# Kernel optimization log

Hardware: AMD Instinct MI355X
Metric: run time of the kernel (lower is better)

The kernel has to match this reference:

```python
import jax, jax.numpy as jnp
import numpy as np

EMBED_DIM = 1024
B, S = 4, 2048
SCALE = float(np.sqrt(EMBED_DIM))


def setup_inputs() -> dict:
    key = jax.random.key(0)
    ks = jax.random.split(key, 9)
    d = EMBED_DIM
    init = 1.0 / np.sqrt(d)
    return {
        "query": jax.random.normal(ks[0], (B, S, d), jnp.float32),
        "key": jax.random.normal(ks[1], (B, S, d), jnp.float32),
        "value": jax.random.normal(ks[2], (B, S, d), jnp.float32),
        "wq": jax.random.uniform(ks[3], (d, d), jnp.float32, -init, init),
        "bq": jax.random.uniform(ks[4], (d,), jnp.float32, -init, init),
        "wk": jax.random.uniform(ks[5], (d, d), jnp.float32, -init, init),
        "bk": jax.random.uniform(ks[6], (d,), jnp.float32, -init, init),
        "wv": jax.random.uniform(ks[7], (d, d), jnp.float32, -init, init),
        "bv": jax.random.uniform(ks[8], (d,), jnp.float32, -init, init),
    }


def reference(query, key, value, wq, bq, wk, bk, wv, bv):
    # Linear projections (torch Linear: x @ W^T + b; here weights stored as [in, out])
    q = query @ wq + bq            # [B,S,D]
    k = key @ wk + bk              # [B,S,D]
    v = value @ wv + bv            # [B,S,D]
    scores = jnp.einsum("bqd,bkd->bqk", q, k) / SCALE   # [B,S,S]
    attn = jax.nn.softmax(scores, axis=-1)
    # dropout in eval mode -> identity
    return jnp.einsum("bqk,bkd->bqd", attn, v)          # [B,S,D]
```

## Files before the change

### kernel.cpp

```cpp
#include <hip/hip_runtime.h>
#include <hip/hip_bf16.h>

typedef __attribute__((ext_vector_type(4))) float   f32x4;
typedef __attribute__((ext_vector_type(8))) __bf16  bf16x8;
typedef __attribute__((ext_vector_type(4))) __bf16  bf16x4;

#define NB 4
#define SS 2048
#define DD 1024

__device__ __forceinline__ void gload_lds16(const void* g, void* l) {
  __builtin_amdgcn_global_load_lds((const __attribute__((address_space(1))) void*)g,
                                   (__attribute__((address_space(3))) void*)l,
                                   16, 0, 0);
}

__global__ __launch_bounds__(256) void cvt_in_kernel(
    const float* __restrict__ q, const float* __restrict__ k,
    const float* __restrict__ v, __bf16* __restrict__ X)
{
  const float* src = blockIdx.z == 0 ? q : (blockIdx.z == 1 ? k : v);
  __bf16* dst = X + (size_t)blockIdx.z * (size_t)(NB * SS * DD);
  size_t i = ((size_t)blockIdx.x * 256 + threadIdx.x) * 4;
  float4 f = *(const float4*)&src[i];
  bf16x4 o = { (__bf16)f.x, (__bf16)f.y, (__bf16)f.z, (__bf16)f.w };
  *(bf16x4*)&dst[i] = o;
}

__global__ __launch_bounds__(256) void prep_w_kernel(
    const float* __restrict__ wq, const float* __restrict__ wk, const float* __restrict__ wv,
    const float* __restrict__ bq, const float* __restrict__ bk, const float* __restrict__ bv,
    __bf16* __restrict__ Wt, float* __restrict__ biasbuf)
{
  const int z = blockIdx.z;
  const float* W  = z == 0 ? wq : (z == 1 ? wk : wv);
  const float* bi = z == 0 ? bq : (z == 1 ? bk : bv);
  __bf16* dst = Wt + (size_t)z * (size_t)(DD * DD);
  const int n0 = blockIdx.x * 32, k0 = blockIdx.y * 32;
  __shared__ float t[32][33];
  const int tx = threadIdx.x & 31, ty = threadIdx.x >> 5;
  #pragma unroll
  for (int i = 0; i < 4; i++)
    t[ty + 8 * i][tx] = W[(size_t)(k0 + ty + 8 * i) * DD + n0 + tx];
  __syncthreads();
  #pragma unroll
  for (int i = 0; i < 4; i++)
    dst[(size_t)(n0 + ty + 8 * i) * DD + k0 + tx] = (__bf16)t[tx][ty + 8 * i];
  if (blockIdx.x == 0 && blockIdx.y == 0) {
    #pragma unroll
    for (int i = 0; i < 4; i++)
      biasbuf[z * DD + threadIdx.x + 256 * i] = bi[threadIdx.x + 256 * i];
  }
}

__global__ __launch_bounds__(256) void transpose_v_kernel(
    const __bf16* __restrict__ V, __bf16* __restrict__ Vt)
{
  const int b = blockIdx.z;
  const int d0 = blockIdx.x * 32, s0 = blockIdx.y * 32;
  __shared__ __bf16 t[32][34];
  const int tx = threadIdx.x & 31, ty = threadIdx.x >> 5;
  const __bf16* src = V + ((size_t)b * SS + s0) * DD + d0;
  #pragma unroll
  for (int i = 0; i < 4; i++)
    t[ty + 8 * i][tx] = src[(size_t)(ty + 8 * i) * DD + tx];
  __syncthreads();
  __bf16* dst = Vt + ((size_t)b * DD + d0) * SS + s0;
  #pragma unroll
  for (int i = 0; i < 4; i++)
    dst[(size_t)(ty + 8 * i) * SS + tx] = t[tx][ty + 8 * i];
}


#define A_OFF(BUF, MH) (((BUF)*2 + (MH)) * 16384)
#define B_OFF(BUF, NH) (65536 + ((BUF)*2 + (NH)) * 16384)

#define STAGE_A(BUF, MH, T) do { int t_ = (T); if (t_ >= NT) t_ = 0;            \
  const __bf16* gs_ = Ablk + (size_t)(MH) * (64 * (size_t)lda) + (size_t)t_ * 64; \
  gload_lds16(gs_ + aoff0, smem + A_OFF(BUF, MH) + tid * 16);                    \
  gload_lds16(gs_ + aoff1, smem + A_OFF(BUF, MH) + 8192 + tid * 16); } while (0)

#define STAGE_B(BUF, NH, T) do { int t_ = (T); if (t_ >= NT) t_ = 0;            \
  const __bf16* gs_ = Bblk + (size_t)(NH) * (32 * (size_t)ldb) + (size_t)t_ * 64; \
  gload_lds16(gs_ + boff0, smem + B_OFF(BUF, NH) + tid * 16);                    \
  gload_lds16(gs_ + boff1, smem + B_OFF(BUF, NH) + 8192 + tid * 16); } while (0)

#define DSREAD_A(DST, BUF, MH)                                                  \
  _Pragma("unroll") for (int mi = 0; mi < 4; ++mi) {                            \
    _Pragma("unroll") for (int ks = 0; ks < 2; ++ks)                            \
      DST[mi][ks] = *(const bf16x8*)(smem + A_OFF(BUF, MH) + arb[ks] + mi * 2048); }

#define DSREAD_B(DST, BUF, NH)                                                  \
  _Pragma("unroll") for (int ni = 0; ni < 2; ++ni) {                            \
    _Pragma("unroll") for (int ks = 0; ks < 2; ++ks)                            \
      DST[ni][ks] = *(const bf16x8*)(smem + B_OFF(BUF, NH) + brb[ks] + ni * 2048); }

#define BARRIER_MFMA(AF, BF, MH, NH) do {                                       \
  __builtin_amdgcn_s_barrier();                                                 \
  asm volatile("s_waitcnt lgkmcnt(0)" ::: "memory");                            \
  __builtin_amdgcn_sched_barrier(0);                                            \
  __builtin_amdgcn_s_setprio(1);                                                \
  _Pragma("unroll") for (int mi = 0; mi < 4; ++mi)                              \
  _Pragma("unroll") for (int ni = 0; ni < 2; ++ni)                              \
  _Pragma("unroll") for (int ks = 0; ks < 2; ++ks)                              \
    acc[(MH)*4+mi][(NH)*2+ni] = __builtin_amdgcn_mfma_f32_16x16x32_bf16(        \
        AF[mi][ks], BF[ni][ks], acc[(MH)*4+mi][(NH)*2+ni], 0, 0, 0);            \
  __builtin_amdgcn_s_setprio(0);                                                \
  __builtin_amdgcn_sched_barrier(0);                                            \
  __builtin_amdgcn_s_barrier(); } while (0)

template <int EPI>
__global__ __launch_bounds__(512) void gemm8p_kernel(
    const __bf16* __restrict__ A, const __bf16* __restrict__ B,
    float scale, void* __restrict__ Cout,
    int K, int lda, int ldb, int ldc,
    long strideA, long strideB, long strideC)
{
  extern __shared__ char smem[];

  const int gx = gridDim.x, gy = gridDim.y;
  const int nwg = gx * gy * gridDim.z;
  int lin = blockIdx.x + gx * (blockIdx.y + gy * blockIdx.z);
  const int cpx = nwg >> 3;
  int swz = (lin & 7) * cpx + (lin >> 3);
  const int bx = swz % gx;
  int rem = swz / gx;
  const int by = rem % gy;
  const int bz = rem / gy;

  const long brow = (long)by * 256, bcol = (long)bx * 256;
  const __bf16* Ablk = A + (size_t)bz * strideA + (size_t)brow * lda;
  const __bf16* Bblk = B + (size_t)bz * strideB + (size_t)bcol * ldb;

  const int tid  = threadIdx.x;
  const int lane = tid & 63;
  const int wid  = tid >> 6;
  const int wm = wid >> 2, wn = wid & 3;
  const int l15 = lane & 15, l4 = lane >> 4;
  const int lx = (lane & 7) << 4;

  const int NT = K >> 6;
  const int niter = NT >> 1;

  int aoff0, aoff1, boff0, boff1;
  #pragma unroll
  for (int i = 0; i < 2; ++i) {
    const int p = i * 8192 + tid * 16;
    const int l = p ^ (((p >> 7) & 7) << 4);
    const int r = p >> 7;
    const int kb = l & 127;
    const int av = ((r >> 6) * 128 + (r & 63)) * lda + (kb >> 1);
    const int bv = ((r >> 5) * 64 + (r & 31)) * ldb + (kb >> 1);
    if (i == 0) { aoff0 = av; boff0 = bv; } else { aoff1 = av; boff1 = bv; }
  }

  int arb[2], brb[2];
  #pragma unroll
  for (int ks = 0; ks < 2; ++ks) {
    arb[ks] = ((((wm * 64 + l15) * 64 + l4 * 8) * 2) + ks * 64) ^ lx;
    brb[ks] = ((((wn * 32 + l15) * 64 + l4 * 8) * 2) + ks * 64) ^ lx;
  }

  f32x4 acc[8][4] = {};
  bf16x8 a0[4][2], a1[4][2], b0[2][2], b1[2][2];

  STAGE_B(0, 0, 0); STAGE_A(0, 0, 0); STAGE_A(0, 1, 0); STAGE_B(0, 1, 0);
  STAGE_B(1, 0, 1); STAGE_A(1, 0, 1);
  asm volatile("s_waitcnt vmcnt(4)" ::: "memory");
  __builtin_amdgcn_s_barrier();

  for (int it = 0; it < niter; ++it) {
    const int tt = it * 2;
    DSREAD_A(a0, 0, 0); DSREAD_B(b0, 0, 0);
    STAGE_A(1, 1, tt + 1);
    BARRIER_MFMA(a0, b0, 0, 0);
    DSREAD_A(a1, 0, 1);
    STAGE_B(1, 1, tt + 1);
    BARRIER_MFMA(a1, b0, 1, 0);
    DSREAD_B(b1, 0, 1);
    STAGE_B(0, 0, tt + 2);
    BARRIER_MFMA(a0, b1, 0, 1);
    STAGE_A(0, 0, tt + 2);
    asm volatile("s_waitcnt vmcnt(4)" ::: "memory");
    BARRIER_MFMA(a1, b1, 1, 1);
    DSREAD_A(a0, 1, 0); DSREAD_B(b0, 1, 0);
    STAGE_A(0, 1, tt + 2);
    BARRIER_MFMA(a0, b0, 0, 0);
    DSREAD_A(a1, 1, 1);
    STAGE_B(0, 1, tt + 2);
    BARRIER_MFMA(a1, b0, 1, 0);
    DSREAD_B(b1, 1, 1);
    STAGE_B(1, 0, tt + 3);
    BARRIER_MFMA(a0, b1, 0, 1);
    STAGE_A(1, 0, tt + 3);
    asm volatile("s_waitcnt vmcnt(4)" ::: "memory");
    BARRIER_MFMA(a1, b1, 1, 1);
  }

  const int cr = l4 * 4;
  __bf16* C = (__bf16*)Cout + (size_t)bz * strideC;
  #pragma unroll
  for (int m = 0; m < 8; ++m) {
    #pragma unroll
    for (int n = 0; n < 4; ++n) {
      const long row = brow + wm * 128 + m * 16 + cr;
      const long col = bcol + wn * 64 + n * 16 + l15;
      #pragma unroll
      for (int e = 0; e < 4; ++e)
        C[(row + e) * (size_t)ldc + col] = (__bf16)__expf(acc[m][n][e] * scale);
    }
  }
}


#define A2_OFF(BUF)      ((BUF) * 16384)
#define B2_OFF(BUF, NH)  (32768 + ((BUF)*2 + (NH)) * 16384)

#define STAGE_SA(BUF, T) do { int t_ = (T); if (t_ >= NT) t_ = 0;              \
  const __bf16* gA_ = Ablk + (size_t)t_ * 64;                                   \
  gload_lds16(gA_ + aoff0, smem + A2_OFF(BUF) + tid * 16);                      \
  gload_lds16(gA_ + aoff1, smem + A2_OFF(BUF) + 8192 + tid * 16);               \
  const __bf16* gB_ = Bblk + (size_t)t_ * 64;                                   \
  gload_lds16(gB_ + boff0, smem + B2_OFF(BUF, 0) + tid * 16);                   \
  gload_lds16(gB_ + boff1, smem + B2_OFF(BUF, 0) + 8192 + tid * 16); } while (0)

#define STAGE_SB(BUF, T) do { int t_ = (T); if (t_ >= NT) t_ = 0;              \
  const __bf16* gB_ = Bblk + (size_t)(128 * (size_t)ldb) + (size_t)t_ * 64;     \
  gload_lds16(gB_ + boff0, smem + B2_OFF(BUF, 1) + tid * 16);                   \
  gload_lds16(gB_ + boff1, smem + B2_OFF(BUF, 1) + 8192 + tid * 16); } while (0)

#define DSREAD_A2(BUF)                                                          \
  _Pragma("unroll") for (int mi = 0; mi < 4; ++mi) {                            \
    _Pragma("unroll") for (int ks = 0; ks < 2; ++ks)                            \
      af[mi][ks] = *(const bf16x8*)(smem + A2_OFF(BUF) + ara[ks] + mi * 2048); }

#define DSREAD_B2(DST, BUF, NH)                                                 \
  _Pragma("unroll") for (int ni = 0; ni < 2; ++ni) {                            \
    _Pragma("unroll") for (int ks = 0; ks < 2; ++ks)                            \
      DST[ni][ks] = *(const bf16x8*)(smem + B2_OFF(BUF, NH) + brb2[ks] + ni * 2048); }

#define MFMA2(BF, NH, DOSUM) do {                                               \
  __builtin_amdgcn_s_barrier();                                                 \
  asm volatile("s_waitcnt lgkmcnt(0)" ::: "memory");                            \
  __builtin_amdgcn_sched_barrier(0);                                            \
  __builtin_amdgcn_s_setprio(1);                                                \
  _Pragma("unroll") for (int mi = 0; mi < 4; ++mi)                              \
  _Pragma("unroll") for (int ni = 0; ni < 2; ++ni)                              \
  _Pragma("unroll") for (int ks = 0; ks < 2; ++ks)                              \
    acc[mi][(NH)*2+ni] = __builtin_amdgcn_mfma_f32_16x16x32_bf16(               \
        af[mi][ks], BF[ni][ks], acc[mi][(NH)*2+ni], 0, 0, 0);                   \
  if constexpr (EPI == 2) { if (DOSUM) {                                        \
    _Pragma("unroll") for (int mi = 0; mi < 4; ++mi)                            \
    _Pragma("unroll") for (int ks = 0; ks < 2; ++ks)                            \
      accs[mi] = __builtin_amdgcn_mfma_f32_16x16x32_bf16(                       \
          af[mi][ks], onesf, accs[mi], 0, 0, 0); } }                            \
  __builtin_amdgcn_s_setprio(0);                                                \
  __builtin_amdgcn_sched_barrier(0);                                            \
  __builtin_amdgcn_s_barrier(); } while (0)

template <int EPI>
__global__ __launch_bounds__(512) void gemm128_kernel(
    const __bf16* __restrict__ A, const __bf16* __restrict__ B,
    const float* __restrict__ bias, void* __restrict__ Cout,
    int K, int lda, int ldb, int ldc,
    long strideA, long strideB, long strideC)
{
  extern __shared__ char smem[];

  const int gx = gridDim.x, gy = gridDim.y;
  const int nwg = gx * gy * gridDim.z;
  int lin = blockIdx.x + gx * (blockIdx.y + gy * blockIdx.z);
  const int cpx = nwg >> 3;
  int swz = (lin & 7) * cpx + (lin >> 3);
  const int bx = swz % gx;
  int rem = swz / gx;
  const int by = rem % gy;
  const int bz = rem / gy;

  const long brow = (long)by * 128, bcol = (long)bx * 256;
  const __bf16* Ablk = A + (size_t)bz * strideA + (size_t)brow * lda;
  const __bf16* Bblk = B + (size_t)bz * strideB + (size_t)bcol * ldb;

  const int tid  = threadIdx.x;
  const int lane = tid & 63;
  const int wid  = tid >> 6;
  const int wm = wid >> 2, wn = wid & 3;
  const int l15 = lane & 15, l4 = lane >> 4;
  const int lx = (lane & 7) << 4;

  const int NT = K >> 6;
  const int niter = NT >> 1;

  int aoff0, aoff1, boff0, boff1;
  #pragma unroll
  for (int i = 0; i < 2; ++i) {
    const int p = i * 8192 + tid * 16;
    const int r = p >> 7;
    const int kb = (p ^ ((r & 7) << 4)) & 127;
    const int av = r * lda + (kb >> 1);
    const int bv = r * ldb + (kb >> 1);
    if (i == 0) { aoff0 = av; boff0 = bv; } else { aoff1 = av; boff1 = bv; }
  }

  int ara[2], brb2[2];
  #pragma unroll
  for (int ks = 0; ks < 2; ++ks) {
    ara[ks]  = ((((wm * 64 + l15) * 64 + l4 * 8) * 2) + ks * 64) ^ lx;
    brb2[ks] = ((((wn * 32 + l15) * 64 + l4 * 8) * 2) + ks * 64) ^ lx;
  }

  f32x4 acc[4][4] = {};
  f32x4 accs[4] = {};
  bf16x8 af[4][2], b0[2][2], b1[2][2];
  bf16x8 onesf;
  #pragma unroll
  for (int j = 0; j < 8; ++j) onesf[j] = (__bf16)1.0f;

  STAGE_SA(0, 0); STAGE_SB(0, 0); STAGE_SA(1, 1);
  asm volatile("s_waitcnt vmcnt(6)" ::: "memory");
  __builtin_amdgcn_s_barrier();

  for (int it = 0; it < niter; ++it) {
    const int tt = it * 2;
    STAGE_SB(1, tt + 1);
    asm volatile("s_waitcnt vmcnt(6)" ::: "memory");
    DSREAD_A2(0); DSREAD_B2(b0, 0, 0);
    MFMA2(b0, 0, 1);
    STAGE_SA(0, tt + 2);
    asm volatile("s_waitcnt vmcnt(6)" ::: "memory");
    DSREAD_B2(b1, 0, 1);
    MFMA2(b1, 1, 0);
    STAGE_SB(0, tt + 2);
    asm volatile("s_waitcnt vmcnt(6)" ::: "memory");
    DSREAD_A2(1); DSREAD_B2(b0, 1, 0);
    MFMA2(b0, 0, 1);
    STAGE_SA(1, tt + 3);
    asm volatile("s_waitcnt vmcnt(6)" ::: "memory");
    DSREAD_B2(b1, 1, 1);
    MFMA2(b1, 1, 0);
  }

  if constexpr (EPI == 2) {
    float* C = (float*)Cout + (size_t)bz * strideC;
    #pragma unroll
    for (int mi = 0; mi < 4; ++mi) {
      f32x4 inv;
      #pragma unroll
      for (int e = 0; e < 4; ++e) inv[e] = 1.0f / accs[mi][e];
      #pragma unroll
      for (int n = 0; n < 4; ++n) {
        const long row = brow + wm * 64 + mi * 16 + l4 * 4;
        const long col = bcol + (n >> 1) * 128 + wn * 32 + (n & 1) * 16 + l15;
        #pragma unroll
        for (int e = 0; e < 4; ++e)
          C[(row + e) * (size_t)ldc + col] = acc[mi][n][e] * inv[e];
      }
    }
  } else {
    __bf16* C = (__bf16*)Cout + (size_t)bz * strideC;
    #pragma unroll
    for (int mi = 0; mi < 4; ++mi) {
      #pragma unroll
      for (int n = 0; n < 4; ++n) {
        const long row = brow + wm * 64 + mi * 16 + l4 * 4;
        const long col = bcol + (n >> 1) * 128 + wn * 32 + (n & 1) * 16 + l15;
        const float bvv = bias[bz * DD + col];
        #pragma unroll
        for (int e = 0; e < 4; ++e)
          C[(row + e) * (size_t)ldc + col] = (__bf16)(acc[mi][n][e] + bvv);
      }
    }
  }
}

extern "C" void kernel_launch(void* const* d_in, const int* in_sizes, int n_in,
                              void* d_out, int out_size, void* d_ws, size_t ws_size,
                              hipStream_t stream)
{
  const float* query = (const float*)d_in[0];
  const float* key   = (const float*)d_in[1];
  const float* value = (const float*)d_in[2];
  const float* wq = (const float*)d_in[3];
  const float* bq = (const float*)d_in[4];
  const float* wk = (const float*)d_in[5];
  const float* bk = (const float*)d_in[6];
  const float* wv = (const float*)d_in[7];
  const float* bv = (const float*)d_in[8];

  char* ws = (char*)d_ws;
  __bf16* Xbf     = (__bf16*)(ws + 0);
  __bf16* Wt      = (__bf16*)(ws + 50331648);
  float*  biasbuf = (float*)(ws + 56623104);
  __bf16* Qb      = (__bf16*)(ws + 56635392);
  __bf16* Kb      = (__bf16*)(ws + 73412608);
  __bf16* Vb      = (__bf16*)(ws + 90189824);
  __bf16* P       = Xbf;
  __bf16* Vt      = Qb;

  hipFuncSetAttribute((const void*)gemm8p_kernel<1>, hipFuncAttributeMaxDynamicSharedMemorySize, 131072);
  hipFuncSetAttribute((const void*)gemm128_kernel<0>, hipFuncAttributeMaxDynamicSharedMemorySize, 131072);
  hipFuncSetAttribute((const void*)gemm128_kernel<2>, hipFuncAttributeMaxDynamicSharedMemorySize, 131072);

  dim3 b256(256), b512(512);

  cvt_in_kernel<<<dim3(8192, 1, 3), b256, 0, stream>>>(query, key, value, Xbf);
  prep_w_kernel<<<dim3(32, 32, 3), b256, 0, stream>>>(wq, wk, wv, bq, bk, bv, Wt, biasbuf);

  gemm128_kernel<0><<<dim3(4, 64, 3), b512, 98304, stream>>>(
      Xbf, Wt, biasbuf, Qb,
      1024, 1024, 1024, 1024,
      8388608L, 1048576L, 8388608L);
  gemm8p_kernel<1><<<dim3(8, 8, 4), b512, 131072, stream>>>(
      Qb, Kb, 0.03125f, P,
      1024, 1024, 1024, 2048,
      2097152L, 2097152L, 4194304L);

  transpose_v_kernel<<<dim3(32, 64, 4), b256, 0, stream>>>(Vb, Vt);

  gemm128_kernel<2><<<dim3(4, 16, 4), b512, 98304, stream>>>(
      P, Vt, nullptr, d_out,
      2048, 2048, 2048, 1024,
      4194304L, 2097152L, 2097152L);

  (void)in_sizes; (void)n_in; (void)out_size; (void)ws_size;
}
```

Baseline: 182.1 us.

## Fuse fp32-to-bf16 input conversion and V transpose into projection GEMM

Adds a dedicated projection kernel that loads fp32 activations directly through registers, converts them to bf16, and writes them into LDS. This removes the separate conversion pass and its bf16 scratch buffer. The V projection epilogue writes its output already transposed, which removes the transpose kernel. This saves two launches and several full-tensor memory round trips. The trade-offs are that the A operand now goes through register-staged loads rather than direct global-to-LDS loads, and the transposed V stores are strided.

Result: faster. 172.2 us (-5.5%).

```diff
diff --git a/kernel.cpp b/kernel.cpp
--- a/kernel.cpp
+++ b/kernel.cpp
@@ -13,18 +13,6 @@
   __builtin_amdgcn_global_load_lds((const __attribute__((address_space(1))) void*)g,
                                    (__attribute__((address_space(3))) void*)l,
                                    16, 0, 0);
-}
-
-__global__ __launch_bounds__(256) void cvt_in_kernel(
-    const float* __restrict__ q, const float* __restrict__ k,
-    const float* __restrict__ v, __bf16* __restrict__ X)
-{
-  const float* src = blockIdx.z == 0 ? q : (blockIdx.z == 1 ? k : v);
-  __bf16* dst = X + (size_t)blockIdx.z * (size_t)(NB * SS * DD);
-  size_t i = ((size_t)blockIdx.x * 256 + threadIdx.x) * 4;
-  float4 f = *(const float4*)&src[i];
-  bf16x4 o = { (__bf16)f.x, (__bf16)f.y, (__bf16)f.z, (__bf16)f.w };
-  *(bf16x4*)&dst[i] = o;
 }
 
 __global__ __launch_bounds__(256) void prep_w_kernel(
@@ -53,22 +41,173 @@
   }
 }
 
-__global__ __launch_bounds__(256) void transpose_v_kernel(
-    const __bf16* __restrict__ V, __bf16* __restrict__ Vt)
+#define A2_OFF(BUF)      ((BUF) * 16384)
+#define B2_OFF(BUF, NH)  (32768 + ((BUF)*2 + (NH)) * 16384)
+
+#define DSREAD_A2(BUF)                                                          \
+  _Pragma("unroll") for (int mi = 0; mi < 4; ++mi) {                            \
+    _Pragma("unroll") for (int ks = 0; ks < 2; ++ks)                            \
+      af[mi][ks] = *(const bf16x8*)(smem + A2_OFF(BUF) + ara[ks] + mi * 2048); }
+
+#define DSREAD_B2(DST, BUF, NH)                                                 \
+  _Pragma("unroll") for (int ni = 0; ni < 2; ++ni) {                            \
+    _Pragma("unroll") for (int ks = 0; ks < 2; ++ks)                            \
+      DST[ni][ks] = *(const bf16x8*)(smem + B2_OFF(BUF, NH) + brb2[ks] + ni * 2048); }
+
+
+#define PJ_GLA(V0, V1, V2, V3, T) do { int t_ = (T); if (t_ >= 16) t_ = 0;      \
+  const float* g_ = Ablk + (size_t)t_ * 64;                                     \
+  V0 = *(const float4*)(g_ + aoffF0); V1 = *(const float4*)(g_ + aoffF0 + 4);   \
+  V2 = *(const float4*)(g_ + aoffF1); V3 = *(const float4*)(g_ + aoffF1 + 4);   \
+  __builtin_amdgcn_sched_barrier(0); } while (0)
+
+#define PJ_WRA(BUF, V0, V1, V2, V3) do {                                        \
+  bf16x8 w0_, w1_;                                                              \
+  w0_[0]=(__bf16)V0.x; w0_[1]=(__bf16)V0.y; w0_[2]=(__bf16)V0.z; w0_[3]=(__bf16)V0.w; \
+  w0_[4]=(__bf16)V1.x; w0_[5]=(__bf16)V1.y; w0_[6]=(__bf16)V1.z; w0_[7]=(__bf16)V1.w; \
+  w1_[0]=(__bf16)V2.x; w1_[1]=(__bf16)V2.y; w1_[2]=(__bf16)V2.z; w1_[3]=(__bf16)V2.w; \
+  w1_[4]=(__bf16)V3.x; w1_[5]=(__bf16)V3.y; w1_[6]=(__bf16)V3.z; w1_[7]=(__bf16)V3.w; \
+  *(bf16x8*)(smem + A2_OFF(BUF) + tid * 16) = w0_;                              \
+  *(bf16x8*)(smem + A2_OFF(BUF) + 8192 + tid * 16) = w1_; } while (0)
+
+#define PJ_SB0(BUF, T) do { int t_ = (T); if (t_ >= 16) t_ = 0;                 \
+  const __bf16* gB_ = Bblk + (size_t)t_ * 64;                                   \
+  gload_lds16(gB_ + boff0, smem + B2_OFF(BUF, 0) + tid * 16);                   \
+  gload_lds16(gB_ + boff1, smem + B2_OFF(BUF, 0) + 8192 + tid * 16); } while (0)
+
+#define PJ_SB1(BUF, T) do { int t_ = (T); if (t_ >= 16) t_ = 0;                 \
+  const __bf16* gB_ = Bblk + (size_t)(128 * 1024) + (size_t)t_ * 64;            \
+  gload_lds16(gB_ + boff0, smem + B2_OFF(BUF, 1) + tid * 16);                   \
+  gload_lds16(gB_ + boff1, smem + B2_OFF(BUF, 1) + 8192 + tid * 16); } while (0)
+
+#define PJ_MFMA(BF, NH) do {                                                    \
+  __builtin_amdgcn_s_barrier();                                                 \
+  asm volatile("s_waitcnt lgkmcnt(0)" ::: "memory");                            \
+  __builtin_amdgcn_sched_barrier(0);                                            \
+  __builtin_amdgcn_s_setprio(1);                                                \
+  _Pragma("unroll") for (int mi = 0; mi < 4; ++mi)                              \
+  _Pragma("unroll") for (int ni = 0; ni < 2; ++ni)                              \
+  _Pragma("unroll") for (int ks = 0; ks < 2; ++ks)                              \
+    acc[mi][(NH)*2+ni] = __builtin_amdgcn_mfma_f32_16x16x32_bf16(               \
+        af[mi][ks], BF[ni][ks], acc[mi][(NH)*2+ni], 0, 0, 0);                   \
+  __builtin_amdgcn_s_setprio(0);                                                \
+  __builtin_amdgcn_sched_barrier(0);                                            \
+  __builtin_amdgcn_s_barrier(); } while (0)
+
+__global__ __launch_bounds__(512) void proj_kernel(
+    const float* __restrict__ Xq, const float* __restrict__ Xk, const float* __restrict__ Xv,
+    const __bf16* __restrict__ Wt, const float* __restrict__ bias,
+    __bf16* __restrict__ Qo, __bf16* __restrict__ Ko, __bf16* __restrict__ Vt)
 {
-  const int b = blockIdx.z;
-  const int d0 = blockIdx.x * 32, s0 = blockIdx.y * 32;
-  __shared__ __bf16 t[32][34];
-  const int tx = threadIdx.x & 31, ty = threadIdx.x >> 5;
-  const __bf16* src = V + ((size_t)b * SS + s0) * DD + d0;
-  #pragma unroll
-  for (int i = 0; i < 4; i++)
-    t[ty + 8 * i][tx] = src[(size_t)(ty + 8 * i) * DD + tx];
-  __syncthreads();
-  __bf16* dst = Vt + ((size_t)b * DD + d0) * SS + s0;
-  #pragma unroll
-  for (int i = 0; i < 4; i++)
-    dst[(size_t)(ty + 8 * i) * SS + tx] = t[tx][ty + 8 * i];
+  extern __shared__ char smem[];
+
+  const int gx = gridDim.x, gy = gridDim.y;
+  const int nwg = gx * gy * gridDim.z;
+  int lin = blockIdx.x + gx * (blockIdx.y + gy * blockIdx.z);
+  const int cpx = nwg >> 3;
+  int swz = (lin & 7) * cpx + (lin >> 3);
+  const int bx = swz % gx;
+  int rem = swz / gx;
+  const int by = rem % gy;
+  const int bz = rem / gy;
+
+  const long brow = (long)by * 128, bcol = (long)bx * 256;
+  const float* Xsel = bz == 0 ? Xq : (bz == 1 ? Xk : Xv);
+  const float* Ablk = Xsel + (size_t)brow * 1024;
+  const __bf16* Bblk = Wt + (size_t)bz * (DD * DD) + (size_t)bcol * 1024;
+
+  const int tid  = threadIdx.x;
+  const int lane = tid & 63;
+  const int wid  = tid >> 6;
+  const int wm = wid >> 2, wn = wid & 3;
+  const int l15 = lane & 15, l4 = lane >> 4;
+  const int lx = (lane & 7) << 4;
+
+  const int niter = 8;
+
+  int aoffF0, aoffF1, boff0, boff1;
+  #pragma unroll
+  for (int i = 0; i < 2; ++i) {
+    const int p = i * 8192 + tid * 16;
+    const int r = p >> 7;
+    const int kb = (p ^ ((r & 7) << 4)) & 127;
+    const int aF = r * 1024 + (kb >> 1);
+    const int bO = r * 1024 + (kb >> 1);
+    if (i == 0) { aoffF0 = aF; boff0 = bO; } else { aoffF1 = aF; boff1 = bO; }
+  }
+
+  int ara[2], brb2[2];
+  #pragma unroll
+  for (int ks = 0; ks < 2; ++ks) {
+    ara[ks]  = ((((wm * 64 + l15) * 64 + l4 * 8) * 2) + ks * 64) ^ lx;
+    brb2[ks] = ((((wn * 32 + l15) * 64 + l4 * 8) * 2) + ks * 64) ^ lx;
+  }
+
+  f32x4 acc[4][4] = {};
+  bf16x8 af[4][2], b0[2][2], b1[2][2];
+  float4 La0, La1, La2, La3, Lb0, Lb1, Lb2, Lb3;
+
+  PJ_GLA(La0, La1, La2, La3, 0);
+  PJ_SB0(0, 0); PJ_SB1(0, 0); PJ_SB0(1, 1);
+  PJ_GLA(Lb0, Lb1, Lb2, Lb3, 1);
+  asm volatile("s_waitcnt vmcnt(10)" ::: "memory");
+  PJ_WRA(0, La0, La1, La2, La3);
+  asm volatile("s_waitcnt vmcnt(0)" ::: "memory");
+  PJ_WRA(1, Lb0, Lb1, Lb2, Lb3);
+  asm volatile("s_waitcnt lgkmcnt(0)" ::: "memory");
+  __builtin_amdgcn_s_barrier();
+
+  for (int it = 0; it < niter; ++it) {
+    const int tt = it * 2;
+    PJ_GLA(La0, La1, La2, La3, tt + 2);
+    PJ_SB1(1, tt + 1);
+    DSREAD_A2(0); DSREAD_B2(b0, 0, 0);
+    PJ_MFMA(b0, 0);
+    asm volatile("s_waitcnt vmcnt(2)" ::: "memory");
+    PJ_WRA(0, La0, La1, La2, La3);
+    PJ_SB0(0, tt + 2);
+    DSREAD_B2(b1, 0, 1);
+    PJ_MFMA(b1, 1);
+    PJ_GLA(Lb0, Lb1, Lb2, Lb3, tt + 3);
+    PJ_SB1(0, tt + 2);
+    DSREAD_A2(1); DSREAD_B2(b0, 1, 0);
+    PJ_MFMA(b0, 0);
+    asm volatile("s_waitcnt vmcnt(2)" ::: "memory");
+    PJ_WRA(1, Lb0, Lb1, Lb2, Lb3);
+    PJ_SB0(1, tt + 3);
+    DSREAD_B2(b1, 1, 1);
+    PJ_MFMA(b1, 1);
+  }
+
+  if (bz == 2) {
+    #pragma unroll
+    for (int mi = 0; mi < 4; ++mi) {
+      #pragma unroll
+      for (int n = 0; n < 4; ++n) {
+        const long row = brow + wm * 64 + mi * 16 + l4 * 4;
+        const long col = bcol + (n >> 1) * 128 + wn * 32 + (n & 1) * 16 + l15;
+        const float bvv = bias[2 * DD + col];
+        const long bb = row >> 11, s = row & 2047;
+        bf16x4 pk = { (__bf16)(acc[mi][n][0] + bvv), (__bf16)(acc[mi][n][1] + bvv),
+                      (__bf16)(acc[mi][n][2] + bvv), (__bf16)(acc[mi][n][3] + bvv) };
+        *(bf16x4*)&Vt[bb * 2097152 + col * 2048 + s] = pk;
+      }
+    }
+  } else {
+    __bf16* C = bz == 0 ? Qo : Ko;
+    #pragma unroll
+    for (int mi = 0; mi < 4; ++mi) {
+      #pragma unroll
+      for (int n = 0; n < 4; ++n) {
+        const long row = brow + wm * 64 + mi * 16 + l4 * 4;
+        const long col = bcol + (n >> 1) * 128 + wn * 32 + (n & 1) * 16 + l15;
+        const float bvv = bias[bz * DD + col];
+        #pragma unroll
+        for (int e = 0; e < 4; ++e)
+          C[(row + e) * 1024 + col] = (__bf16)(acc[mi][n][e] + bvv);
+      }
+    }
+  }
 }
 
 
@@ -109,7 +248,6 @@
   __builtin_amdgcn_sched_barrier(0);                                            \
   __builtin_amdgcn_s_barrier(); } while (0)
 
-template <int EPI>
 __global__ __launch_bounds__(512) void gemm8p_kernel(
     const __bf16* __restrict__ A, const __bf16* __restrict__ B,
     float scale, void* __restrict__ Cout,
@@ -213,9 +351,6 @@
 }
 
 
-#define A2_OFF(BUF)      ((BUF) * 16384)
-#define B2_OFF(BUF, NH)  (32768 + ((BUF)*2 + (NH)) * 16384)
-
 #define STAGE_SA(BUF, T) do { int t_ = (T); if (t_ >= NT) t_ = 0;              \
   const __bf16* gA_ = Ablk + (size_t)t_ * 64;                                   \
   gload_lds16(gA_ + aoff0, smem + A2_OFF(BUF) + tid * 16);                      \
@@ -228,16 +363,6 @@
   const __bf16* gB_ = Bblk + (size_t)(128 * (size_t)ldb) + (size_t)t_ * 64;     \
   gload_lds16(gB_ + boff0, smem + B2_OFF(BUF, 1) + tid * 16);                   \
   gload_lds16(gB_ + boff1, smem + B2_OFF(BUF, 1) + 8192 + tid * 16); } while (0)
-
-#define DSREAD_A2(BUF)                                                          \
-  _Pragma("unroll") for (int mi = 0; mi < 4; ++mi) {                            \
-    _Pragma("unroll") for (int ks = 0; ks < 2; ++ks)                            \
-      af[mi][ks] = *(const bf16x8*)(smem + A2_OFF(BUF) + ara[ks] + mi * 2048); }
-
-#define DSREAD_B2(DST, BUF, NH)                                                 \
-  _Pragma("unroll") for (int ni = 0; ni < 2; ++ni) {                            \
-    _Pragma("unroll") for (int ks = 0; ks < 2; ++ks)                            \
-      DST[ni][ks] = *(const bf16x8*)(smem + B2_OFF(BUF, NH) + brb2[ks] + ni * 2048); }
 
 #define MFMA2(BF, NH, DOSUM) do {                                               \
   __builtin_amdgcn_s_barrier();                                                 \
@@ -249,19 +374,18 @@
   _Pragma("unroll") for (int ks = 0; ks < 2; ++ks)                              \
     acc[mi][(NH)*2+ni] = __builtin_amdgcn_mfma_f32_16x16x32_bf16(               \
         af[mi][ks], BF[ni][ks], acc[mi][(NH)*2+ni], 0, 0, 0);                   \
-  if constexpr (EPI == 2) { if (DOSUM) {                                        \
+  if (DOSUM) {                                                                  \
     _Pragma("unroll") for (int mi = 0; mi < 4; ++mi)                            \
     _Pragma("unroll") for (int ks = 0; ks < 2; ++ks)                            \
       accs[mi] = __builtin_amdgcn_mfma_f32_16x16x32_bf16(                       \
-          af[mi][ks], onesf, accs[mi], 0, 0, 0); } }                            \
+          af[mi][ks], onesf, accs[mi], 0, 0, 0); }                              \
   __builtin_amdgcn_s_setprio(0);                                                \
   __builtin_amdgcn_sched_barrier(0);                                            \
   __builtin_amdgcn_s_barrier(); } while (0)
 
-template <int EPI>
 __global__ __launch_bounds__(512) void gemm128_kernel(
     const __bf16* __restrict__ A, const __bf16* __restrict__ B,
-    const float* __restrict__ bias, void* __restrict__ Cout,
+    void* __restrict__ Cout,
     int K, int lda, int ldb, int ldc,
     long strideA, long strideB, long strideC)
 {
@@ -340,35 +464,19 @@
     MFMA2(b1, 1, 0);
   }
 
-  if constexpr (EPI == 2) {
-    float* C = (float*)Cout + (size_t)bz * strideC;
+  float* C = (float*)Cout + (size_t)bz * strideC;
+  #pragma unroll
+  for (int mi = 0; mi < 4; ++mi) {
+    f32x4 inv;
     #pragma unroll
-    for (int mi = 0; mi < 4; ++mi) {
-      f32x4 inv;
+    for (int e = 0; e < 4; ++e) inv[e] = 1.0f / accs[mi][e];
+    #pragma unroll
+    for (int n = 0; n < 4; ++n) {
+      const long row = brow + wm * 64 + mi * 16 + l4 * 4;
+      const long col = bcol + (n >> 1) * 128 + wn * 32 + (n & 1) * 16 + l15;
       #pragma unroll
-      for (int e = 0; e < 4; ++e) inv[e] = 1.0f / accs[mi][e];
-      #pragma unroll
-      for (int n = 0; n < 4; ++n) {
-        const long row = brow + wm * 64 + mi * 16 + l4 * 4;
-        const long col = bcol + (n >> 1) * 128 + wn * 32 + (n & 1) * 16 + l15;
-        #pragma unroll
-        for (int e = 0; e < 4; ++e)
-          C[(row + e) * (size_t)ldc + col] = acc[mi][n][e] * inv[e];
-      }
-    }
-  } else {
-    __bf16* C = (__bf16*)Cout + (size_t)bz * strideC;
-    #pragma unroll
-    for (int mi = 0; mi < 4; ++mi) {
-      #pragma unroll
-      for (int n = 0; n < 4; ++n) {
-        const long row = brow + wm * 64 + mi * 16 + l4 * 4;
-        const long col = bcol + (n >> 1) * 128 + wn * 32 + (n & 1) * 16 + l15;
-        const float bvv = bias[bz * DD + col];
-        #pragma unroll
-        for (int e = 0; e < 4; ++e)
-          C[(row + e) * (size_t)ldc + col] = (__bf16)(acc[mi][n][e] + bvv);
-      }
+      for (int e = 0; e < 4; ++e)
+        C[(row + e) * (size_t)ldc + col] = acc[mi][n][e] * inv[e];
     }
   }
 }
@@ -388,37 +496,31 @@
   const float* bv = (const float*)d_in[8];
 
   char* ws = (char*)d_ws;
-  __bf16* Xbf     = (__bf16*)(ws + 0);
-  __bf16* Wt      = (__bf16*)(ws + 50331648);
-  float*  biasbuf = (float*)(ws + 56623104);
-  __bf16* Qb      = (__bf16*)(ws + 56635392);
-  __bf16* Kb      = (__bf16*)(ws + 73412608);
-  __bf16* Vb      = (__bf16*)(ws + 90189824);
-  __bf16* P       = Xbf;
-  __bf16* Vt      = Qb;
-
-  hipFuncSetAttribute((const void*)gemm8p_kernel<1>, hipFuncAttributeMaxDynamicSharedMemorySize, 131072);
-  hipFuncSetAttribute((const void*)gemm128_kernel<0>, hipFuncAttributeMaxDynamicSharedMemorySize, 131072);
-  hipFuncSetAttribute((const void*)gemm128_kernel<2>, hipFuncAttributeMaxDynamicSharedMemorySize, 131072);
+  __bf16* P       = (__bf16*)(ws + 0);
+  __bf16* Wt      = (__bf16*)(ws + 33554432);
+  float*  biasbuf = (float*)(ws + 39845888);
+  __bf16* Qb      = (__bf16*)(ws + 39858176);
+  __bf16* Kb      = (__bf16*)(ws + 56635392);
+  __bf16* Vt      = (__bf16*)(ws + 73412608);
+
+  hipFuncSetAttribute((const void*)proj_kernel,    hipFuncAttributeMaxDynamicSharedMemorySize, 131072);
+  hipFuncSetAttribute((const void*)gemm8p_kernel,  hipFuncAttributeMaxDynamicSharedMemorySize, 131072);
+  hipFuncSetAttribute((const void*)gemm128_kernel, hipFuncAttributeMaxDynamicSharedMemorySize, 131072);
 
   dim3 b256(256), b512(512);
 
-  cvt_in_kernel<<<dim3(8192, 1, 3), b256, 0, stream>>>(query, key, value, Xbf);
   prep_w_kernel<<<dim3(32, 32, 3), b256, 0, stream>>>(wq, wk, wv, bq, bk, bv, Wt, biasbuf);
 
-  gemm128_kernel<0><<<dim3(4, 64, 3), b512, 98304, stream>>>(
-      Xbf, Wt, biasbuf, Qb,
-      1024, 1024, 1024, 1024,
-      8388608L, 1048576L, 8388608L);
-  gemm8p_kernel<1><<<dim3(8, 8, 4), b512, 131072, stream>>>(
+  proj_kernel<<<dim3(4, 64, 3), b512, 98304, stream>>>(
+      query, key, value, Wt, biasbuf, Qb, Kb, Vt);
+
+  gemm8p_kernel<<<dim3(8, 8, 4), b512, 131072, stream>>>(
       Qb, Kb, 0.03125f, P,
       1024, 1024, 1024, 2048,
       2097152L, 2097152L, 4194304L);
 
-  transpose_v_kernel<<<dim3(32, 64, 4), b256, 0, stream>>>(Vb, Vt);
-
-  gemm128_kernel<2><<<dim3(4, 16, 4), b512, 98304, stream>>>(
-      P, Vt, nullptr, d_out,
+  gemm128_kernel<<<dim3(4, 16, 4), b512, 98304, stream>>>(
+      P, Vt, d_out,
       2048, 2048, 2048, 1024,
       4194304L, 2097152L, 2097152L);
 
```

## Fuse V transpose into projection epilogue and use 128x128 two-block GEMM

Applied to the files above, without the earlier changes.

Replaces the 128x256 512-thread GEMM with a 128x128 256-thread kernel that uses a simple double-buffered loop and launch bounds allowing two blocks per CU. The V projection epilogue now writes its output transposed straight into the Vt buffer, which removes the separate transpose kernel and its extra read and write of V. The transposed stores are strided 8-byte writes, which may coalesce poorly, and the smaller tiles lower data reuse per block.

Result: faster. 168.9 us (-7.2%).

```diff
diff --git a/kernel.cpp b/kernel.cpp
--- a/kernel.cpp
+++ b/kernel.cpp
@@ -53,22 +53,173 @@
   }
 }
 
-__global__ __launch_bounds__(256) void transpose_v_kernel(
-    const __bf16* __restrict__ V, __bf16* __restrict__ Vt)
+
+#define G2A(BUF) ((BUF) * 16384)
+#define G2B(BUF) (32768 + (BUF) * 16384)
+
+#define G2_STAGE(BUF, T) do { int t_ = (T); if (t_ >= NT) t_ = 0;               \
+  const __bf16* gA_ = Ablk + (size_t)t_ * 64;                                   \
+  const __bf16* gB_ = Bblk + (size_t)t_ * 64;                                   \
+  gload_lds16(gA_ + o0, smem + G2A(BUF) + tid * 16);                            \
+  gload_lds16(gA_ + o1, smem + G2A(BUF) + 4096 + tid * 16);                     \
+  gload_lds16(gA_ + o2, smem + G2A(BUF) + 8192 + tid * 16);                     \
+  gload_lds16(gA_ + o3, smem + G2A(BUF) + 12288 + tid * 16);                    \
+  gload_lds16(gB_ + o0, smem + G2B(BUF) + tid * 16);                            \
+  gload_lds16(gB_ + o1, smem + G2B(BUF) + 4096 + tid * 16);                     \
+  gload_lds16(gB_ + o2, smem + G2B(BUF) + 8192 + tid * 16);                     \
+  gload_lds16(gB_ + o3, smem + G2B(BUF) + 12288 + tid * 16); } while (0)
+
+template <int EPI>
+__global__ __launch_bounds__(256, 2) void gemm2b_kernel(
+    const __bf16* __restrict__ A, const __bf16* __restrict__ B,
+    const float* __restrict__ bias, float* __restrict__ Fout,
+    __bf16* __restrict__ Qo, __bf16* __restrict__ Ko, __bf16* __restrict__ Vt,
+    int K, int lda, int ldb, int ldc,
+    long strideA, long strideB, long strideC)
 {
-  const int b = blockIdx.z;
-  const int d0 = blockIdx.x * 32, s0 = blockIdx.y * 32;
-  __shared__ __bf16 t[32][34];
-  const int tx = threadIdx.x & 31, ty = threadIdx.x >> 5;
-  const __bf16* src = V + ((size_t)b * SS + s0) * DD + d0;
-  #pragma unroll
-  for (int i = 0; i < 4; i++)
-    t[ty + 8 * i][tx] = src[(size_t)(ty + 8 * i) * DD + tx];
-  __syncthreads();
-  __bf16* dst = Vt + ((size_t)b * DD + d0) * SS + s0;
-  #pragma unroll
-  for (int i = 0; i < 4; i++)
-    dst[(size_t)(ty + 8 * i) * SS + tx] = t[tx][ty + 8 * i];
+  extern __shared__ char smem[];
+
+  const int gx = gridDim.x, gy = gridDim.y;
+  const int nwg = gx * gy * gridDim.z;
+  int lin = blockIdx.x + gx * (blockIdx.y + gy * blockIdx.z);
+  const int cpx = nwg >> 3;
+  int swz = (lin & 7) * cpx + (lin >> 3);
+  const int bx = swz % gx;
+  int rem = swz / gx;
+  const int by = rem % gy;
+  const int bz = rem / gy;
+
+  const long brow = (long)by * 128, bcol = (long)bx * 128;
+  const __bf16* Ablk = A + (size_t)bz * strideA + (size_t)brow * lda;
+  const __bf16* Bblk = B + (size_t)bz * strideB + (size_t)bcol * ldb;
+
+  const int tid  = threadIdx.x;
+  const int lane = tid & 63;
+  const int wid  = tid >> 6;
+  const int wm = wid >> 1, wn = wid & 1;
+  const int l15 = lane & 15, l4 = lane >> 4;
+  const int lx = (lane & 7) << 4;
+
+  const int NT = K >> 6;
+
+  int o0, o1, o2, o3;
+  #pragma unroll
+  for (int i = 0; i < 4; ++i) {
+    const int p = i * 4096 + tid * 16;
+    const int r = p >> 7;
+    const int kb = (p ^ ((r & 7) << 4)) & 127;
+    const int off = r * lda + (kb >> 1);
+    if (i == 0) o0 = off; else if (i == 1) o1 = off;
+    else if (i == 2) o2 = off; else o3 = off;
+  }
+
+  int ara[2], brb[2];
+  #pragma unroll
+  for (int ks = 0; ks < 2; ++ks) {
+    ara[ks] = ((((wm * 64 + l15) * 64 + l4 * 8) * 2) + ks * 64) ^ lx;
+    brb[ks] = ((((wn * 64 + l15) * 64 + l4 * 8) * 2) + ks * 64) ^ lx;
+  }
+
+  f32x4 acc[4][4] = {};
+  f32x4 accs[4] = {};
+  bf16x8 af[4][2], bf[4][2];
+  bf16x8 onesf;
+  #pragma unroll
+  for (int j = 0; j < 8; ++j) onesf[j] = (__bf16)1.0f;
+
+  G2_STAGE(0, 0);
+  G2_STAGE(1, 1);
+  asm volatile("s_waitcnt vmcnt(8)" ::: "memory");
+  __builtin_amdgcn_s_barrier();
+
+  for (int t = 0; t < NT; ++t) {
+    const int cur = t & 1;
+    const int abase = cur * 16384;
+    const int bbase = 32768 + cur * 16384;
+    #pragma unroll
+    for (int mi = 0; mi < 4; ++mi)
+      #pragma unroll
+      for (int ks = 0; ks < 2; ++ks)
+        af[mi][ks] = *(const bf16x8*)(smem + abase + ara[ks] + mi * 2048);
+    #pragma unroll
+    for (int ni = 0; ni < 4; ++ni)
+      #pragma unroll
+      for (int ks = 0; ks < 2; ++ks)
+        bf[ni][ks] = *(const bf16x8*)(smem + bbase + brb[ks] + ni * 2048);
+    asm volatile("s_waitcnt lgkmcnt(0)" ::: "memory");
+    __builtin_amdgcn_sched_barrier(0);
+    __builtin_amdgcn_s_barrier();
+    G2_STAGE(cur, t + 2);
+    __builtin_amdgcn_s_setprio(1);
+    #pragma unroll
+    for (int mi = 0; mi < 4; ++mi)
+      #pragma unroll
+      for (int ni = 0; ni < 4; ++ni)
+        #pragma unroll
+        for (int ks = 0; ks < 2; ++ks)
+          acc[mi][ni] = __builtin_amdgcn_mfma_f32_16x16x32_bf16(
+              af[mi][ks], bf[ni][ks], acc[mi][ni], 0, 0, 0);
+    if constexpr (EPI == 2) {
+      #pragma unroll
+      for (int mi = 0; mi < 4; ++mi)
+        #pragma unroll
+        for (int ks = 0; ks < 2; ++ks)
+          accs[mi] = __builtin_amdgcn_mfma_f32_16x16x32_bf16(
+              af[mi][ks], onesf, accs[mi], 0, 0, 0);
+    }
+    __builtin_amdgcn_s_setprio(0);
+    __builtin_amdgcn_sched_barrier(0);
+    asm volatile("s_waitcnt vmcnt(8)" ::: "memory");
+    __builtin_amdgcn_s_barrier();
+  }
+
+  if constexpr (EPI == 2) {
+    float* C = Fout + (size_t)bz * strideC;
+    #pragma unroll
+    for (int mi = 0; mi < 4; ++mi) {
+      f32x4 inv;
+      #pragma unroll
+      for (int e = 0; e < 4; ++e) inv[e] = 1.0f / accs[mi][e];
+      #pragma unroll
+      for (int ni = 0; ni < 4; ++ni) {
+        const long row = brow + wm * 64 + mi * 16 + l4 * 4;
+        const long col = bcol + wn * 64 + ni * 16 + l15;
+        #pragma unroll
+        for (int e = 0; e < 4; ++e)
+          C[(row + e) * (size_t)ldc + col] = acc[mi][ni][e] * inv[e];
+      }
+    }
+  } else {
+    if (bz == 2) {
+      #pragma unroll
+      for (int mi = 0; mi < 4; ++mi) {
+        #pragma unroll
+        for (int ni = 0; ni < 4; ++ni) {
+          const long row = brow + wm * 64 + mi * 16 + l4 * 4;
+          const long col = bcol + wn * 64 + ni * 16 + l15;
+          const float bvv = bias[2 * DD + col];
+          const long bb = row >> 11, s = row & 2047;
+          bf16x4 pk = { (__bf16)(acc[mi][ni][0] + bvv), (__bf16)(acc[mi][ni][1] + bvv),
+                        (__bf16)(acc[mi][ni][2] + bvv), (__bf16)(acc[mi][ni][3] + bvv) };
+          *(bf16x4*)&Vt[bb * 2097152 + col * 2048 + s] = pk;
+        }
+      }
+    } else {
+      __bf16* C = bz == 0 ? Qo : Ko;
+      #pragma unroll
+      for (int mi = 0; mi < 4; ++mi) {
+        #pragma unroll
+        for (int ni = 0; ni < 4; ++ni) {
+          const long row = brow + wm * 64 + mi * 16 + l4 * 4;
+          const long col = bcol + wn * 64 + ni * 16 + l15;
+          const float bvv = bias[bz * DD + col];
+          #pragma unroll
+          for (int e = 0; e < 4; ++e)
+            C[(row + e) * 1024 + col] = (__bf16)(acc[mi][ni][e] + bvv);
+        }
+      }
+    }
+  }
 }
 
 
@@ -90,7 +241,7 @@
     _Pragma("unroll") for (int ks = 0; ks < 2; ++ks)                            \
       DST[mi][ks] = *(const bf16x8*)(smem + A_OFF(BUF, MH) + arb[ks] + mi * 2048); }
 
-#define DSREAD_B(DST, BUF, NH)                                                  \
+#define DSREAD_BS(DST, BUF, NH)                                                 \
   _Pragma("unroll") for (int ni = 0; ni < 2; ++ni) {                            \
     _Pragma("unroll") for (int ks = 0; ks < 2; ++ks)                            \
       DST[ni][ks] = *(const bf16x8*)(smem + B_OFF(BUF, NH) + brb[ks] + ni * 2048); }
@@ -109,7 +260,6 @@
   __builtin_amdgcn_sched_barrier(0);                                            \
   __builtin_amdgcn_s_barrier(); } while (0)
 
-template <int EPI>
 __global__ __launch_bounds__(512) void gemm8p_kernel(
     const __bf16* __restrict__ A, const __bf16* __restrict__ B,
     float scale, void* __restrict__ Cout,
@@ -171,25 +321,25 @@
 
   for (int it = 0; it < niter; ++it) {
     const int tt = it * 2;
-    DSREAD_A(a0, 0, 0); DSREAD_B(b0, 0, 0);
+    DSREAD_A(a0, 0, 0); DSREAD_BS(b0, 0, 0);
     STAGE_A(1, 1, tt + 1);
     BARRIER_MFMA(a0, b0, 0, 0);
     DSREAD_A(a1, 0, 1);
     STAGE_B(1, 1, tt + 1);
     BARRIER_MFMA(a1, b0, 1, 0);
-    DSREAD_B(b1, 0, 1);
+    DSREAD_BS(b1, 0, 1);
     STAGE_B(0, 0, tt + 2);
     BARRIER_MFMA(a0, b1, 0, 1);
     STAGE_A(0, 0, tt + 2);
     asm volatile("s_waitcnt vmcnt(4)" ::: "memory");
     BARRIER_MFMA(a1, b1, 1, 1);
-    DSREAD_A(a0, 1, 0); DSREAD_B(b0, 1, 0);
+    DSREAD_A(a0, 1, 0); DSREAD_BS(b0, 1, 0);
     STAGE_A(0, 1, tt + 2);
     BARRIER_MFMA(a0, b0, 0, 0);
     DSREAD_A(a1, 1, 1);
     STAGE_B(0, 1, tt + 2);
     BARRIER_MFMA(a1, b0, 1, 0);
-    DSREAD_B(b1, 1, 1);
+    DSREAD_BS(b1, 1, 1);
     STAGE_B(1, 0, tt + 3);
     BARRIER_MFMA(a0, b1, 0, 1);
     STAGE_A(1, 0, tt + 3);
@@ -208,167 +358,6 @@
       #pragma unroll
       for (int e = 0; e < 4; ++e)
         C[(row + e) * (size_t)ldc + col] = (__bf16)__expf(acc[m][n][e] * scale);
-    }
-  }
-}
-
-
-#define A2_OFF(BUF)      ((BUF) * 16384)
-#define B2_OFF(BUF, NH)  (32768 + ((BUF)*2 + (NH)) * 16384)
-
-#define STAGE_SA(BUF, T) do { int t_ = (T); if (t_ >= NT) t_ = 0;              \
-  const __bf16* gA_ = Ablk + (size_t)t_ * 64;                                   \
-  gload_lds16(gA_ + aoff0, smem + A2_OFF(BUF) + tid * 16);                      \
-  gload_lds16(gA_ + aoff1, smem + A2_OFF(BUF) + 8192 + tid * 16);               \
-  const __bf16* gB_ = Bblk + (size_t)t_ * 64;                                   \
-  gload_lds16(gB_ + boff0, smem + B2_OFF(BUF, 0) + tid * 16);                   \
-  gload_lds16(gB_ + boff1, smem + B2_OFF(BUF, 0) + 8192 + tid * 16); } while (0)
-
-#define STAGE_SB(BUF, T) do { int t_ = (T); if (t_ >= NT) t_ = 0;              \
-  const __bf16* gB_ = Bblk + (size_t)(128 * (size_t)ldb) + (size_t)t_ * 64;     \
-  gload_lds16(gB_ + boff0, smem + B2_OFF(BUF, 1) + tid * 16);                   \
-  gload_lds16(gB_ + boff1, smem + B2_OFF(BUF, 1) + 8192 + tid * 16); } while (0)
-
-#define DSREAD_A2(BUF)                                                          \
-  _Pragma("unroll") for (int mi = 0; mi < 4; ++mi) {                            \
-    _Pragma("unroll") for (int ks = 0; ks < 2; ++ks)                            \
-      af[mi][ks] = *(const bf16x8*)(smem + A2_OFF(BUF) + ara[ks] + mi * 2048); }
-
-#define DSREAD_B2(DST, BUF, NH)                                                 \
-  _Pragma("unroll") for (int ni = 0; ni < 2; ++ni) {                            \
-    _Pragma("unroll") for (int ks = 0; ks < 2; ++ks)                            \
-      DST[ni][ks] = *(const bf16x8*)(smem + B2_OFF(BUF, NH) + brb2[ks] + ni * 2048); }
-
-#define MFMA2(BF, NH, DOSUM) do {                                               \
-  __builtin_amdgcn_s_barrier();                                                 \
-  asm volatile("s_waitcnt lgkmcnt(0)" ::: "memory");                            \
-  __builtin_amdgcn_sched_barrier(0);                                            \
-  __builtin_amdgcn_s_setprio(1);                                                \
-  _Pragma("unroll") for (int mi = 0; mi < 4; ++mi)                              \
-  _Pragma("unroll") for (int ni = 0; ni < 2; ++ni)                              \
-  _Pragma("unroll") for (int ks = 0; ks < 2; ++ks)                              \
-    acc[mi][(NH)*2+ni] = __builtin_amdgcn_mfma_f32_16x16x32_bf16(               \
-        af[mi][ks], BF[ni][ks], acc[mi][(NH)*2+ni], 0, 0, 0);                   \
-  if constexpr (EPI == 2) { if (DOSUM) {                                        \
-    _Pragma("unroll") for (int mi = 0; mi < 4; ++mi)                            \
-    _Pragma("unroll") for (int ks = 0; ks < 2; ++ks)                            \
-      accs[mi] = __builtin_amdgcn_mfma_f32_16x16x32_bf16(                       \
-          af[mi][ks], onesf, accs[mi], 0, 0, 0); } }                            \
-  __builtin_amdgcn_s_setprio(0);                                                \
-  __builtin_amdgcn_sched_barrier(0);                                            \
-  __builtin_amdgcn_s_barrier(); } while (0)
-
-template <int EPI>
-__global__ __launch_bounds__(512) void gemm128_kernel(
-    const __bf16* __restrict__ A, const __bf16* __restrict__ B,
-    const float* __restrict__ bias, void* __restrict__ Cout,
-    int K, int lda, int ldb, int ldc,
-    long strideA, long strideB, long strideC)
-{
-  extern __shared__ char smem[];
-
-  const int gx = gridDim.x, gy = gridDim.y;
-  const int nwg = gx * gy * gridDim.z;
-  int lin = blockIdx.x + gx * (blockIdx.y + gy * blockIdx.z);
-  const int cpx = nwg >> 3;
-  int swz = (lin & 7) * cpx + (lin >> 3);
-  const int bx = swz % gx;
-  int rem = swz / gx;
-  const int by = rem % gy;
-  const int bz = rem / gy;
-
-  const long brow = (long)by * 128, bcol = (long)bx * 256;
-  const __bf16* Ablk = A + (size_t)bz * strideA + (size_t)brow * lda;
-  const __bf16* Bblk = B + (size_t)bz * strideB + (size_t)bcol * ldb;
-
-  const int tid  = threadIdx.x;
-  const int lane = tid & 63;
-  const int wid  = tid >> 6;
-  const int wm = wid >> 2, wn = wid & 3;
-  const int l15 = lane & 15, l4 = lane >> 4;
-  const int lx = (lane & 7) << 4;
-
-  const int NT = K >> 6;
-  const int niter = NT >> 1;
-
-  int aoff0, aoff1, boff0, boff1;
-  #pragma unroll
-  for (int i = 0; i < 2; ++i) {
-    const int p = i * 8192 + tid * 16;
-    const int r = p >> 7;
-    const int kb = (p ^ ((r & 7) << 4)) & 127;
-    const int av = r * lda + (kb >> 1);
-    const int bv = r * ldb + (kb >> 1);
-    if (i == 0) { aoff0 = av; boff0 = bv; } else { aoff1 = av; boff1 = bv; }
-  }
-
-  int ara[2], brb2[2];
-  #pragma unroll
-  for (int ks = 0; ks < 2; ++ks) {
-    ara[ks]  = ((((wm * 64 + l15) * 64 + l4 * 8) * 2) + ks * 64) ^ lx;
-    brb2[ks] = ((((wn * 32 + l15) * 64 + l4 * 8) * 2) + ks * 64) ^ lx;
-  }
-
-  f32x4 acc[4][4] = {};
-  f32x4 accs[4] = {};
-  bf16x8 af[4][2], b0[2][2], b1[2][2];
-  bf16x8 onesf;
-  #pragma unroll
-  for (int j = 0; j < 8; ++j) onesf[j] = (__bf16)1.0f;
-
-  STAGE_SA(0, 0); STAGE_SB(0, 0); STAGE_SA(1, 1);
-  asm volatile("s_waitcnt vmcnt(6)" ::: "memory");
-  __builtin_amdgcn_s_barrier();
-
-  for (int it = 0; it < niter; ++it) {
-    const int tt = it * 2;
-    STAGE_SB(1, tt + 1);
-    asm volatile("s_waitcnt vmcnt(6)" ::: "memory");
-    DSREAD_A2(0); DSREAD_B2(b0, 0, 0);
-    MFMA2(b0, 0, 1);
-    STAGE_SA(0, tt + 2);
-    asm volatile("s_waitcnt vmcnt(6)" ::: "memory");
-    DSREAD_B2(b1, 0, 1);
-    MFMA2(b1, 1, 0);
-    STAGE_SB(0, tt + 2);
-    asm volatile("s_waitcnt vmcnt(6)" ::: "memory");
-    DSREAD_A2(1); DSREAD_B2(b0, 1, 0);
-    MFMA2(b0, 0, 1);
-    STAGE_SA(1, tt + 3);
-    asm volatile("s_waitcnt vmcnt(6)" ::: "memory");
-    DSREAD_B2(b1, 1, 1);
-    MFMA2(b1, 1, 0);
-  }
-
-  if constexpr (EPI == 2) {
-    float* C = (float*)Cout + (size_t)bz * strideC;
-    #pragma unroll
-    for (int mi = 0; mi < 4; ++mi) {
-      f32x4 inv;
-      #pragma unroll
-      for (int e = 0; e < 4; ++e) inv[e] = 1.0f / accs[mi][e];
-      #pragma unroll
-      for (int n = 0; n < 4; ++n) {
-        const long row = brow + wm * 64 + mi * 16 + l4 * 4;
-        const long col = bcol + (n >> 1) * 128 + wn * 32 + (n & 1) * 16 + l15;
-        #pragma unroll
-        for (int e = 0; e < 4; ++e)
-          C[(row + e) * (size_t)ldc + col] = acc[mi][n][e] * inv[e];
-      }
-    }
-  } else {
-    __bf16* C = (__bf16*)Cout + (size_t)bz * strideC;
-    #pragma unroll
-    for (int mi = 0; mi < 4; ++mi) {
-      #pragma unroll
-      for (int n = 0; n < 4; ++n) {
-        const long row = brow + wm * 64 + mi * 16 + l4 * 4;
-        const long col = bcol + (n >> 1) * 128 + wn * 32 + (n & 1) * 16 + l15;
-        const float bvv = bias[bz * DD + col];
-        #pragma unroll
-        for (int e = 0; e < 4; ++e)
-          C[(row + e) * (size_t)ldc + col] = (__bf16)(acc[mi][n][e] + bvv);
-      }
     }
   }
 }
@@ -393,32 +382,27 @@
   float*  biasbuf = (float*)(ws + 56623104);
   __bf16* Qb      = (__bf16*)(ws + 56635392);
   __bf16* Kb      = (__bf16*)(ws + 73412608);
-  __bf16* Vb      = (__bf16*)(ws + 90189824);
+  __bf16* Vt      = (__bf16*)(ws + 90189824);
   __bf16* P       = Xbf;
-  __bf16* Vt      = Qb;
-
-  hipFuncSetAttribute((const void*)gemm8p_kernel<1>, hipFuncAttributeMaxDynamicSharedMemorySize, 131072);
-  hipFuncSetAttribute((const void*)gemm128_kernel<0>, hipFuncAttributeMaxDynamicSharedMemorySize, 131072);
-  hipFuncSetAttribute((const void*)gemm128_kernel<2>, hipFuncAttributeMaxDynamicSharedMemorySize, 131072);
+
+  hipFuncSetAttribute((const void*)gemm2b_kernel<0>, hipFuncAttributeMaxDynamicSharedMemorySize, 65536);
+  hipFuncSetAttribute((const void*)gemm2b_kernel<2>, hipFuncAttributeMaxDynamicSharedMemorySize, 65536);
+  hipFuncSetAttribute((const void*)gemm8p_kernel,    hipFuncAttributeMaxDynamicSharedMemorySize, 131072);
 
   dim3 b256(256), b512(512);
 
   cvt_in_kernel<<<dim3(8192, 1, 3), b256, 0, stream>>>(query, key, value, Xbf);
   prep_w_kernel<<<dim3(32, 32, 3), b256, 0, stream>>>(wq, wk, wv, bq, bk, bv, Wt, biasbuf);
-
-  gemm128_kernel<0><<<dim3(4, 64, 3), b512, 98304, stream>>>(
-      Xbf, Wt, biasbuf, Qb,
+  gemm2b_kernel<0><<<dim3(8, 64, 3), b256, 65536, stream>>>(
+      Xbf, Wt, biasbuf, nullptr, Qb, Kb, Vt,
       1024, 1024, 1024, 1024,
-      8388608L, 1048576L, 8388608L);
-  gemm8p_kernel<1><<<dim3(8, 8, 4), b512, 131072, stream>>>(
+      8388608L, 1048576L, 0L);
+  gemm8p_kernel<<<dim3(8, 8, 4), b512, 131072, stream>>>(
       Qb, Kb, 0.03125f, P,
       1024, 1024, 1024, 2048,
       2097152L, 2097152L, 4194304L);
-
-  transpose_v_kernel<<<dim3(32, 64, 4), b256, 0, stream>>>(Vb, Vt);
-
-  gemm128_kernel<2><<<dim3(4, 16, 4), b512, 98304, stream>>>(
-      P, Vt, nullptr, d_out,
+  gemm2b_kernel<2><<<dim3(8, 16, 4), b256, 65536, stream>>>(
+      P, Vt, nullptr, (float*)d_out, nullptr, nullptr, nullptr,
       2048, 2048, 2048, 1024,
       4194304L, 2097152L, 2097152L);
 
```
